# Kernel tuning notes

Measured on AMD Instinct MI355X. Metric: run time of the kernel, lower is better.

## Reference

```python
import jax, jax.numpy as jnp
import numpy as np

IMAGE_SIZE = 128
B = 2048
PI = float(np.pi)


def setup_inputs() -> dict:
    key = jax.random.key(0)
    k1, k2, k3 = jax.random.split(key, 3)
    W = jax.random.normal(k1, (B, 16), dtype=jnp.float32)
    noise_gauss = jax.random.normal(k2, (B, IMAGE_SIZE, IMAGE_SIZE), dtype=jnp.float32)
    noise_uniform = jax.random.uniform(k3, (B, IMAGE_SIZE, IMAGE_SIZE), dtype=jnp.float32)
    return {"W": W, "noise_gauss": noise_gauss, "noise_uniform": noise_uniform}


def _decode(W, noise_gauss, noise_uniform):
    H = IMAGE_SIZE
    cx = cy = H // 2
    xx, yy = jnp.meshgrid(jnp.arange(H, dtype=jnp.float32),
                          jnp.arange(H, dtype=jnp.float32), indexing="ij")  # (H,H)

    def w(k):
        return W[:, k][:, None, None]  # (B,1,1) for broadcasting over pixels

    r = jnp.sqrt((xx - cx) ** 2 + (yy - cy) ** 2)  # (H,H)

    # disk
    img = jnp.clip(w(0) * 6 - r, 0.0, 1.0)  # (B,H,H)

    # central square (mask replaces dynamic slice img[cy-half:cy+half, cx-half:cx+half])
    half = jnp.floor(jnp.clip(jnp.abs(w(1)) * 8 + 2, 2, 12))
    square = ((xx >= cy - half) & (xx < cy + half) &
              (yy >= cx - half) & (yy < cx + half)).astype(jnp.float32)
    img = img + 0.5 * square

    # sinusoids
    img = img + 0.5 * jnp.sin(w(2) * 2 * PI * xx / H)
    img = img + 0.5 * jnp.sin(w(3) * 2 * PI * yy / H)
    diag = (xx + yy) / 2
    img = img + 0.5 * jnp.sin(w(4) * PI * diag / H)
    img = img + 0.5 * jnp.sin((yy + w(5) * 10) * PI / H)

    # brightness offset
    img = img + w(6)

    # gaussian blob (int() truncates toward zero)
    off = jnp.trunc(w(7) * 5)
    bx = cx + off
    by = cy + off
    sigma = 4 + jnp.abs(w(7)) * 5
    img = img + jnp.exp(-((xx - bx) ** 2 + (yy - by) ** 2) / (2 * sigma ** 2))

    # ring
    img = img + ((r - w(8) * 10) ** 2 < 10).astype(jnp.float32)

    # checkerboard
    cb_size = jnp.floor(jnp.clip(jnp.abs(w(9)) * 8 + 2, 2, 16))
    cb = (jnp.floor(xx / cb_size) + jnp.floor(yy / cb_size)) % 2 * 0.3
    img = img + cb

    # rotated line
    angle = w(10) * PI
    rot_line = jnp.cos(angle) * (xx - cx) + jnp.sin(angle) * (yy - cy)
    img = img + (jnp.abs(rot_line) < 3).astype(jnp.float32) * 0.6

    # angular sinusoid
    theta = jnp.arctan2(yy - cy, xx - cx)
    img = img + 0.5 * jnp.sin(theta * w(11) * 4)

    # noise
    img = img + noise_gauss * 0.2 * w(12)
    img = img + (noise_uniform - 0.5) * w(13) * 0.2

    # contrast + optional inversion
    img = (img - 0.5) * (1 + w(14)) + 0.5
    img = jnp.where(w(15) > 0, 1.0 - img, img)

    # per-image min/max normalization
    mn = jnp.min(img, axis=(1, 2), keepdims=True)
    mx = jnp.max(img, axis=(1, 2), keepdims=True)
    img = (img - mn) / (mx - mn + 1e-8)
    return img[:, None, :, :]  # (B,1,H,W)


def reference(W, noise_gauss, noise_uniform):
    return _decode(W, noise_gauss, noise_uniform)
```

## Files before the change

### kernel.cpp

```cpp
#include <hip/hip_runtime.h>

#define IMG_H   128
#define NPIX    (IMG_H * IMG_H)
#define TPB     512
#define VITERS  (NPIX / (TPB * 4))
#define NWAVES  (TPB / 64)

__device__ __forceinline__ float fast_atan2f(float y, float x) {
    float ax = fabsf(x), ay = fabsf(y);
    float mx = fmaxf(fmaxf(ax, ay), 1e-30f);
    float mn = fminf(ax, ay);
    float a  = mn * __builtin_amdgcn_rcpf(mx);
    float t  = a * a;
    float r  = fmaf(t, fmaf(t, fmaf(t, fmaf(t, 0.0208351f, -0.0851330f),
                                    0.1801410f), -0.3302995f), 0.9998660f);
    r = a * r;
    if (ay > ax)  r = 1.5707963268f - r;
    if (x < 0.0f) r = 3.1415926536f - r;
    return copysignf(r, y);
}

__global__ __launch_bounds__(TPB)
void decode_kernel(const float* __restrict__ W,
                   const float* __restrict__ ng,
                   const float* __restrict__ nu,
                   float* __restrict__ out)
{
    const int b   = blockIdx.x;
    const int tid = threadIdx.x;
    const float* Wb = W + (size_t)b * 16;

    const float w0  = Wb[0],  w1  = Wb[1],  w2  = Wb[2],  w3  = Wb[3];
    const float w4  = Wb[4],  w5  = Wb[5],  w6  = Wb[6],  w7  = Wb[7];
    const float w8  = Wb[8],  w9  = Wb[9],  w10 = Wb[10], w11 = Wb[11];
    const float w12 = Wb[12], w13 = Wb[13], w14 = Wb[14], w15 = Wb[15];

    const float PI    = 3.14159265358979323846f;
    const float PI128 = PI / 128.0f;

    const float cdisk = w0 * 6.0f;
    const float half  = floorf(fminf(fmaxf(fabsf(w1) * 8.0f + 2.0f, 2.0f), 12.0f));
    const float lo    = 64.0f - half, hi = 64.0f + half;
    const float s2    = w2 * (PI / 64.0f);
    const float s3    = w3 * (PI / 64.0f);
    const float s4    = w4 * (PI / 256.0f);
    const float c5    = w5 * 10.0f * PI128;
    const float off7  = truncf(w7 * 5.0f);
    const float bxy   = 64.0f + off7;
    const float sig   = 4.0f + fabsf(w7) * 5.0f;
    const float nb    = -1.0f / (2.0f * sig * sig);
    const float r8    = w8 * 10.0f;
    const float cbs   = floorf(fminf(fmaxf(fabsf(w9) * 8.0f + 2.0f, 2.0f), 16.0f));
    const float icbs  = 1.0f / cbs;
    const float ca    = cosf(w10 * PI);
    const float sa    = sinf(w10 * PI);
    const float a11   = w11 * 4.0f;
    const float n12   = 0.2f * w12;
    const float n13   = 0.2f * w13;
    const float con2  = (w15 > 0.0f) ? -(1.0f + w14) : (1.0f + w14);

    const float4* ng4  = (const float4*)(ng  + (size_t)b * NPIX);
    const float4* nu4  = (const float4*)(nu  + (size_t)b * NPIX);
    float4*       out4 = (float4*)(out + (size_t)b * NPIX);

    float4 vals[VITERS];
    float vmin =  3.402823466e38f;
    float vmax = -3.402823466e38f;

    #pragma unroll
    for (int k = 0; k < VITERS; ++k) {
        const int p4 = k * TPB + tid;
        const int p  = p4 * 4;
        const int i  = p >> 7;
        const int j0 = p & 127;
        const float fi = (float)i;

        const float4 g = ng4[p4];
        const float4 u = nu4[p4];
        const float gg[4] = {g.x, g.y, g.z, g.w};
        const float uu[4] = {u.x, u.y, u.z, u.w};

        const float dx     = fi - 64.0f;
        const float rowsin = 0.5f * __sinf(s2 * fi);
        const bool  mi     = (fi >= lo) && (fi < hi);
        const float ci     = floorf((fi + 0.25f) * icbs);
        const float dxb    = fi - bxy;
        const float dxb2   = dxb * dxb;

        float vout[4];
        #pragma unroll
        for (int q = 0; q < 4; ++q) {
            const float fj = (float)(j0 + q);
            const float dy = fj - 64.0f;
            const float r2 = fmaf(dx, dx, dy * dy);
            const float r  = sqrtf(r2);

            float v = fminf(fmaxf(cdisk - r, 0.0f), 1.0f);
            if (mi && (fj >= lo) && (fj < hi)) v += 0.5f;
            v += rowsin;
            v += 0.5f * __sinf(s3 * fj);
            v += 0.5f * __sinf(s4 * (fi + fj));
            v += 0.5f * __sinf(fmaf(fj, PI128, c5));
            v += w6;
            const float dyb = fj - bxy;
            v += __expf(nb * fmaf(dyb, dyb, dxb2));
            const float tr = r - r8;
            if (tr * tr < 10.0f) v += 1.0f;
            const float cj = floorf((fj + 0.25f) * icbs);
            if (((int)(ci + cj)) & 1) v += 0.3f;
            const float rot = ca * dx + sa * dy;
            if (fabsf(rot) < 3.0f) v += 0.6f;
            const float theta = fast_atan2f(dy, dx);
            v += 0.5f * __sinf(theta * a11);
            v = fmaf(gg[q], n12, v);
            v = fmaf(uu[q] - 0.5f, n13, v);
            v = fmaf(v - 0.5f, con2, 0.5f);

            vout[q] = v;
            vmin = fminf(vmin, v);
            vmax = fmaxf(vmax, v);
        }
        vals[k] = make_float4(vout[0], vout[1], vout[2], vout[3]);
    }

    #pragma unroll
    for (int off = 32; off > 0; off >>= 1) {
        vmin = fminf(vmin, __shfl_xor(vmin, off, 64));
        vmax = fmaxf(vmax, __shfl_xor(vmax, off, 64));
    }

    __shared__ float smin[NWAVES], smax[NWAVES];
    const int wave = tid >> 6;
    if ((tid & 63) == 0) { smin[wave] = vmin; smax[wave] = vmax; }
    __syncthreads();
    float bmin = smin[0], bmax = smax[0];
    #pragma unroll
    for (int wv = 1; wv < NWAVES; ++wv) {
        bmin = fminf(bmin, smin[wv]);
        bmax = fmaxf(bmax, smax[wv]);
    }

    const float scale = 1.0f / (bmax - bmin + 1e-8f);

    #pragma unroll
    for (int k = 0; k < VITERS; ++k) {
        const int p4 = k * TPB + tid;
        float4 v = vals[k];
        v.x = (v.x - bmin) * scale;
        v.y = (v.y - bmin) * scale;
        v.z = (v.z - bmin) * scale;
        v.w = (v.w - bmin) * scale;
        out4[p4] = v;
    }
}

extern "C" void kernel_launch(void* const* d_in, const int* in_sizes, int n_in,
                              void* d_out, int out_size, void* d_ws, size_t ws_size,
                              hipStream_t stream) {
    const float* W  = (const float*)d_in[0];
    const float* ng = (const float*)d_in[1];
    const float* nu = (const float*)d_in[2];
    float* out = (float*)d_out;
    const int B = in_sizes[0] / 16;
    decode_kernel<<<dim3(B), dim3(TPB), 0, stream>>>(W, ng, nu, out);
}
```

Measured before the change: 314.6 us.

## Precompute separable row/column terms in LDS and use nontemporal noise loads

Each block first builds per-row and per-column tables in shared memory: the sinusoids, the Gaussian factors, the square mask, checkerboard parity and the diagonal sine split into sin/cos products. The per-pixel loop then combines these with FMAs instead of calling several transcendentals per pixel. Noise loads are software-pipelined one iteration ahead and use nontemporal loads and stores. This adds an extra __syncthreads and LDS traffic, and uses the angle-addition identity for the diagonal sine, which changes rounding slightly.

```diff
diff --git a/kernel.cpp b/kernel.cpp
--- a/kernel.cpp
+++ b/kernel.cpp
@@ -5,6 +5,8 @@
 #define TPB     512
 #define VITERS  (NPIX / (TPB * 4))
 #define NWAVES  (TPB / 64)
+
+typedef float vfloat4 __attribute__((ext_vector_type(4)));
 
 __device__ __forceinline__ float fast_atan2f(float y, float x) {
     float ax = fabsf(x), ay = fabsf(y);
@@ -58,69 +60,109 @@
     const float n12   = 0.2f * w12;
     const float n13   = 0.2f * w13;
     const float con2  = (w15 > 0.0f) ? -(1.0f + w14) : (1.0f + w14);
-
-    const float4* ng4  = (const float4*)(ng  + (size_t)b * NPIX);
-    const float4* nu4  = (const float4*)(nu  + (size_t)b * NPIX);
-    float4*       out4 = (float4*)(out + (size_t)b * NPIX);
-
-    float4 vals[VITERS];
+    const float ccon  = 0.5f - 0.5f * con2;
+
+    __shared__ float4 colA[IMG_H], colB[IMG_H], rowA[IMG_H], rowB[IMG_H];
+    __shared__ float  smin[NWAVES], smax[NWAVES];
+
+    if (tid < 128) {
+        const float fj  = (float)tid;
+        const float dy  = fj - 64.0f;
+        const float dyb = fj - bxy;
+        const float c0 = 0.5f * __sinf(s3 * fj)
+                       + 0.5f * __sinf(fmaf(fj, PI128, c5))
+                       + w6 - 0.5f * n13;
+        const float cexp = __expf(nb * dyb * dyb);
+        const float csq  = ((fj >= lo) && (fj < hi)) ? 0.5f : 0.0f;
+        const float cj   = floorf((fj + 0.25f) * icbs);
+        const float cpar = (float)(((int)cj) & 1);
+        const int   sw   = tid ^ ((tid >> 3) & 7);
+        colA[sw] = make_float4(c0, cexp, csq, cpar);
+        colB[sw] = make_float4(0.5f * __sinf(s4 * fj), 0.5f * __cosf(s4 * fj), dy, dy * dy);
+    } else if (tid < 256) {
+        const int   i   = tid - 128;
+        const float fi  = (float)i;
+        const float dx  = fi - 64.0f;
+        const float dxb = fi - bxy;
+        const float mi_f = ((fi >= lo) && (fi < hi)) ? 1.0f : 0.0f;
+        const float ci   = floorf((fi + 0.25f) * icbs);
+        const float rpar = (float)(((int)ci) & 1);
+        rowA[i] = make_float4(dx, dx * dx, __expf(nb * dxb * dxb), mi_f);
+        rowB[i] = make_float4(rpar, 0.5f * __sinf(s2 * fi), __sinf(s4 * fi), __cosf(s4 * fi));
+    }
+    __syncthreads();
+
+    const vfloat4* ng4  = (const vfloat4*)(ng  + (size_t)b * NPIX);
+    const vfloat4* nu4  = (const vfloat4*)(nu  + (size_t)b * NPIX);
+    vfloat4*       out4 = (vfloat4*)(out + (size_t)b * NPIX);
+
+    const int i0 = tid >> 5;
+    const int j0 = (tid & 31) << 2;
+
+    float4 cA[4], cB[4];
+    #pragma unroll
+    for (int q = 0; q < 4; ++q) {
+        const int sw = (j0 + q) ^ ((j0 >> 3) & 7);
+        cA[q] = colA[sw];
+        cB[q] = colB[sw];
+    }
+
+    vfloat4 vals[VITERS];
     float vmin =  3.402823466e38f;
     float vmax = -3.402823466e38f;
 
+    vfloat4 gc = __builtin_nontemporal_load(ng4 + tid);
+    vfloat4 uc = __builtin_nontemporal_load(nu4 + tid);
+
     #pragma unroll
     for (int k = 0; k < VITERS; ++k) {
-        const int p4 = k * TPB + tid;
-        const int p  = p4 * 4;
-        const int i  = p >> 7;
-        const int j0 = p & 127;
-        const float fi = (float)i;
-
-        const float4 g = ng4[p4];
-        const float4 u = nu4[p4];
-        const float gg[4] = {g.x, g.y, g.z, g.w};
-        const float uu[4] = {u.x, u.y, u.z, u.w};
-
-        const float dx     = fi - 64.0f;
-        const float rowsin = 0.5f * __sinf(s2 * fi);
-        const bool  mi     = (fi >= lo) && (fi < hi);
-        const float ci     = floorf((fi + 0.25f) * icbs);
-        const float dxb    = fi - bxy;
-        const float dxb2   = dxb * dxb;
+        vfloat4 gn = gc, un = uc;
+        if (k + 1 < VITERS) {
+            gn = __builtin_nontemporal_load(ng4 + (k + 1) * TPB + tid);
+            un = __builtin_nontemporal_load(nu4 + (k + 1) * TPB + tid);
+        }
+
+        const int    i  = i0 + 16 * k;
+        const float4 ra = rowA[i];
+        const float4 rb = rowB[i];
+        const float  dx  = ra.x;
+        const float  rr  = ca * dx;
+
+        const float gg[4] = {gc.x, gc.y, gc.z, gc.w};
+        const float uu[4] = {uc.x, uc.y, uc.z, uc.w};
 
         float vout[4];
         #pragma unroll
         for (int q = 0; q < 4; ++q) {
-            const float fj = (float)(j0 + q);
-            const float dy = fj - 64.0f;
-            const float r2 = fmaf(dx, dx, dy * dy);
-            const float r  = sqrtf(r2);
+            const float dy  = cB[q].z;
+            const float r2  = ra.y + cB[q].w;
+            const float r   = sqrtf(r2);
 
             float v = fminf(fmaxf(cdisk - r, 0.0f), 1.0f);
-            if (mi && (fj >= lo) && (fj < hi)) v += 0.5f;
-            v += rowsin;
-            v += 0.5f * __sinf(s3 * fj);
-            v += 0.5f * __sinf(s4 * (fi + fj));
-            v += 0.5f * __sinf(fmaf(fj, PI128, c5));
-            v += w6;
-            const float dyb = fj - bxy;
-            v += __expf(nb * fmaf(dyb, dyb, dxb2));
+            v += cA[q].x;
+            v += rb.y;
+            v = fmaf(ra.w, cA[q].z, v);
+            v = fmaf(rb.z, cB[q].y, v);
+            v = fmaf(rb.w, cB[q].x, v);
+            v = fmaf(ra.z, cA[q].y, v);
             const float tr = r - r8;
             if (tr * tr < 10.0f) v += 1.0f;
-            const float cj = floorf((fj + 0.25f) * icbs);
-            if (((int)(ci + cj)) & 1) v += 0.3f;
-            const float rot = ca * dx + sa * dy;
+            v = fmaf(fabsf(rb.x - cA[q].w), 0.3f, v);
+            const float rot = fmaf(sa, dy, rr);
             if (fabsf(rot) < 3.0f) v += 0.6f;
             const float theta = fast_atan2f(dy, dx);
-            v += 0.5f * __sinf(theta * a11);
+            v = fmaf(0.5f, __sinf(theta * a11), v);
             v = fmaf(gg[q], n12, v);
-            v = fmaf(uu[q] - 0.5f, n13, v);
-            v = fmaf(v - 0.5f, con2, 0.5f);
+            v = fmaf(uu[q], n13, v);
+            v = fmaf(v, con2, ccon);
 
             vout[q] = v;
             vmin = fminf(vmin, v);
             vmax = fmaxf(vmax, v);
         }
-        vals[k] = make_float4(vout[0], vout[1], vout[2], vout[3]);
+        vfloat4 vv; vv.x = vout[0]; vv.y = vout[1]; vv.z = vout[2]; vv.w = vout[3];
+        vals[k] = vv;
+        gc = gn; uc = un;
     }
 
     #pragma unroll
@@ -129,7 +171,6 @@
         vmax = fmaxf(vmax, __shfl_xor(vmax, off, 64));
     }
 
-    __shared__ float smin[NWAVES], smax[NWAVES];
     const int wave = tid >> 6;
     if ((tid & 63) == 0) { smin[wave] = vmin; smax[wave] = vmax; }
     __syncthreads();
@@ -144,13 +185,12 @@
 
     #pragma unroll
     for (int k = 0; k < VITERS; ++k) {
-        const int p4 = k * TPB + tid;
-        float4 v = vals[k];
+        vfloat4 v = vals[k];
         v.x = (v.x - bmin) * scale;
         v.y = (v.y - bmin) * scale;
         v.z = (v.z - bmin) * scale;
         v.w = (v.w - bmin) * scale;
-        out4[p4] = v;
+        __builtin_nontemporal_store(v, out4 + k * TPB + tid);
     }
 }
 
```

Result: slower. 329.6 us (+4.7%).
